# Performance work log

Measured on AMD Instinct MI355X. Metric: run time of the kernel, lower is better.

The kernel has to match this reference:

```python
import jax, jax.numpy as jnp
import numpy as np

B, C, O, H, W = 4, 64, 64, 128, 128
KH = KW = 3
K = KH * KW  # 9 kernel positions
MRM = 10.0   # max_residue_magnitude


def setup_inputs() -> dict:
    key = jax.random.key(0)
    ks = jax.random.split(key, 6)
    return {
        "x_main": jax.random.normal(ks[0], (B, C, H, W), jnp.float32),
        "x_extra": jax.random.normal(ks[1], (B, C, H, W), jnp.float32),
        "pre_offset": jax.random.normal(ks[2], (B, K, H, W, 2), jnp.float32) * 2.0,
        "pre_sim": jax.random.uniform(ks[3], (B, K, H, W), jnp.float32),
        "weight": jax.random.normal(ks[4], (O, C, KH, KW), jnp.float32) / np.sqrt(C * K),
        "bias": jnp.zeros((O,), jnp.float32),
        "w_om": jax.random.normal(ks[5], (3 * K, C, KH, KW), jnp.float32) * 0.01,
        "b_om": jnp.zeros((3 * K,), jnp.float32),
    }


def _bilinear(img, py, px):
    """img: [C,Hi,Wi]; py, px: [K,Ho,Wo] float sample coords. Zero padding outside."""
    Hi, Wi = img.shape[1], img.shape[2]
    y0 = jnp.floor(py)
    x0 = jnp.floor(px)
    dy = py - y0  # [K,Ho,Wo]
    dx = px - x0

    def gather(yi, xi):
        valid = ((yi >= 0) & (yi <= Hi - 1) & (xi >= 0) & (xi <= Wi - 1)).astype(img.dtype)
        yc = jnp.clip(yi, 0, Hi - 1).astype(jnp.int32)
        xc = jnp.clip(xi, 0, Wi - 1).astype(jnp.int32)
        return img[:, yc, xc] * valid[None]  # [C,K,Ho,Wo]

    v00 = gather(y0, x0)
    v01 = gather(y0, x0 + 1)
    v10 = gather(y0 + 1, x0)
    v11 = gather(y0 + 1, x0 + 1)
    return (v00 * (1 - dy) * (1 - dx) + v01 * (1 - dy) * dx
            + v10 * dy * (1 - dx) + v11 * dy * dx)


def reference(x_main, x_extra, pre_offset, pre_sim, weight, bias, w_om, b_om):
    # conv_offset_mask: 3x3, stride 1, pad 1 -> [B, 3K, H, W]
    out = jax.lax.conv_general_dilated(
        x_extra, w_om, (1, 1), ((1, 1), (1, 1)),
        dimension_numbers=("NCHW", "OIHW", "NCHW")) + b_om[None, :, None, None]
    o1, o2, mask = jnp.split(out, 3, axis=1)  # each [B,K,H,W]
    offset = MRM * jnp.tanh(jnp.concatenate([o1, o2], axis=1))  # [B,2K,H,W]
    # pre_offset reorder: even channels <- pre_offset[...,1] (y), odd <- pre_offset[...,0] (x)
    off_y = offset[:, 0::2] + pre_offset[..., 1]  # [B,K,H,W]
    off_x = offset[:, 1::2] + pre_offset[..., 0]
    mask = jax.nn.sigmoid(mask * pre_sim)  # use_sim=True

    f32 = offset.dtype
    ky = (jnp.arange(K) // KW).astype(f32)  # kernel row per position k
    kx = (jnp.arange(K) % KW).astype(f32)   # kernel col per position k
    # base grid: p = out_pos*stride - pad + k*dil = h - 1 + ky (stride=1,pad=1,dil=1)
    py = off_y + (jnp.arange(H, dtype=f32)[None, None, :, None] - 1.0) + ky[None, :, None, None]
    px = off_x + (jnp.arange(W, dtype=f32)[None, None, None, :] - 1.0) + kx[None, :, None, None]

    sampled = jax.vmap(_bilinear)(x_main, py, px)      # [B,C,K,H,W]
    sampled = sampled * mask[:, None]                   # modulated (DCNv2)
    y = jnp.einsum("bckhw,ock->bohw", sampled, weight.reshape(O, C, K))
    return y + bias[None, :, None, None]
```

## Files before the change

kernel.cpp:

```cpp
#include <hip/hip_runtime.h>
#include <math.h>

#define Bn 4
#define Cn 64
#define On 64
#define Hn 128
#define Wn 128
#define Kn 9
#define HWn (Hn*Wn)
#define ZROW 16384
#define XBSTRIDE (16385*64)

typedef _Float16 v8h __attribute__((ext_vector_type(8)));
typedef float v4f __attribute__((ext_vector_type(4)));

__device__ inline unsigned short f2h(float f) {
  _Float16 h = (_Float16)f;
  return __builtin_bit_cast(unsigned short, h);
}
__device__ inline _Float16 u2h(unsigned v) {
  return __builtin_bit_cast(_Float16, (unsigned short)(v & 0xffff));
}
__device__ inline v8h sp8(_Float16 x) { v8h v = {x,x,x,x,x,x,x,x}; return v; }

__device__ inline void gld_lds16(const void* g, void* s) {
  __builtin_amdgcn_global_load_lds(
      (const __attribute__((address_space(1))) unsigned int*)g,
      (__attribute__((address_space(3))) unsigned int*)s, 16, 0, 0);
}

__global__ __launch_bounds__(256) void k_prep(
    const float* __restrict__ x_main,
    const float* __restrict__ x_extra,
    const float* __restrict__ weight,
    const float* __restrict__ w_om,
    _Float16* __restrict__ xT,
    _Float16* __restrict__ xeF,
    _Float16* __restrict__ Wfrag,
    _Float16* __restrict__ WOMfrag)
{
  const int blk = blockIdx.x;
  const int t = threadIdx.x;

  if (blk < 2048) {
    __shared__ float tile[64 * 65];
    int isExtra = blk >> 10;
    int b  = (blk >> 8) & 3;
    int p0 = (blk & 255) << 6;
    const float* src = (isExtra ? x_extra : x_main) + b * Cn * HWn + p0;
    #pragma unroll
    for (int i = 0; i < 4; ++i) {
      int c  = i * 16 + (t >> 4);
      int p4 = (t & 15) * 4;
      float4 v = *(const float4*)(src + c * HWn + p4);
      tile[c * 65 + p4 + 0] = v.x;
      tile[c * 65 + p4 + 1] = v.y;
      tile[c * 65 + p4 + 2] = v.z;
      tile[c * 65 + p4 + 3] = v.w;
    }
    __syncthreads();
    _Float16* dst = (isExtra ? xeF : xT) + b * XBSTRIDE + p0 * 64;
    int q  = t & 7;
    int pr = t >> 3;
    #pragma unroll
    for (int i = 0; i < 2; ++i) {
      int p = i * 32 + pr;
      v8h pk;
      #pragma unroll
      for (int j = 0; j < 8; ++j)
        pk[j] = (_Float16)tile[(q * 8 + j) * 65 + p];
      *(v8h*)(dst + p * 64 + q * 8) = pk;
    }
  } else {
    int rb = blk - 2048;
    for (int idx = rb * 256 + t; idx < 36864; idx += 64 * 256) {
      int j  = idx & 7;
      int ln = (idx >> 3) & 63;
      int ot = (idx >> 9) & 3;
      int hk = (idx >> 11) & 1;
      int k  = idx >> 12;
      int o = ot * 16 + (ln & 15);
      int c = hk * 32 + (ln >> 4) * 8 + j;
      Wfrag[idx] = (_Float16)weight[(o * Cn + c) * Kn + k];
    }
    for (int idx = rb * 256 + t; idx < 18432; idx += 64 * 256) {
      int j    = idx & 7;
      int ln   = (idx >> 3) & 63;
      int jt   = (idx >> 9) & 1;
      int half = (idx >> 10) & 1;
      int k9   = idx >> 11;
      int jo = jt * 16 + (ln & 15);
      int c  = half * 32 + (ln >> 4) * 8 + j;
      float v = (jo < 27) ? w_om[(jo * Cn + c) * Kn + k9] : 0.f;
      WOMfrag[idx] = (_Float16)v;
    }
    if (rb == 0 && t < 256) {
      int b = t >> 6, c = t & 63;
      xT[b * XBSTRIDE + ZROW * 64 + c] = (_Float16)0.f;
      xeF[b * XBSTRIDE + ZROW * 64 + c] = (_Float16)0.f;
    }
  }
}

__global__ __launch_bounds__(256, 4) void k_fused(
    const _Float16* __restrict__ xT,
    const _Float16* __restrict__ xeF,
    const _Float16* __restrict__ Wfrag,
    const _Float16* __restrict__ WOMfrag,
    const float* __restrict__ pre_offset,
    const float* __restrict__ pre_sim,
    const float* __restrict__ b_om,
    const float* __restrict__ bias,
    float* __restrict__ out)
{
  __shared__ __align__(16) char smem[36864];

  const int t    = threadIdx.x;
  const int lane = t & 63;
  const int wv   = __builtin_amdgcn_readfirstlane(t >> 6);
  const int raw  = blockIdx.x;
  const int blk  = ((raw & 7) << 7) | (raw >> 3);
  const int b    = blk >> 8;
  const int h    = (blk >> 1) & 127;
  const int wq   = (blk & 1) * 4 + wv;
  const int kq   = lane >> 4;
  const int n    = lane & 15;
  const int w    = wq * 16 + n;

  unsigned tapoff[9];
  #pragma unroll
  for (int k9 = 0; k9 < 9; ++k9) {
    int r  = h - 1 + k9 / 3;
    int cc = w - 1 + k9 % 3;
    bool v = ((unsigned)r < (unsigned)Hn) & ((unsigned)cc < (unsigned)Wn);
    tapoff[k9] = (v ? (unsigned)(r * Wn + cc) : (unsigned)ZROW) * 64u;
  }

  const _Float16* xe = xeF + b * XBSTRIDE;
  v4f ca0 = {0,0,0,0}, ca1 = {0,0,0,0};

  {
    const v8h* WomV = (const v8h*)WOMfrag;
    #pragma unroll
    for (int f = 0; f < 9; ++f) {
      int id = wv * 9 + f;
      gld_lds16(WomV + id * 64 + lane, smem + id * 1024);
    }
  }
  __builtin_amdgcn_sched_barrier(0);
  v8h Bt0 = *(const v8h*)(xe + tapoff[0] + kq * 8);
  v8h Bt1 = *(const v8h*)(xe + tapoff[0] + 32 + kq * 8);
  asm volatile("s_waitcnt vmcnt(2)" ::: "memory");
  __builtin_amdgcn_s_barrier();

  #pragma unroll
  for (int k9 = 0; k9 < 9; ++k9) {
    v8h Bn0, Bn1;
    if (k9 < 8) {
      Bn0 = *(const v8h*)(xe + tapoff[k9 + 1] + kq * 8);
      Bn1 = *(const v8h*)(xe + tapoff[k9 + 1] + 32 + kq * 8);
    }
    __builtin_amdgcn_sched_barrier(0);
    const char* fb = smem + k9 * 4096 + lane * 16;
    v8h A00 = *(const v8h*)(fb);
    v8h A01 = *(const v8h*)(fb + 1024);
    ca0 = __builtin_amdgcn_mfma_f32_16x16x32_f16(A00, Bt0, ca0, 0, 0, 0);
    ca1 = __builtin_amdgcn_mfma_f32_16x16x32_f16(A01, Bt0, ca1, 0, 0, 0);
    v8h A10 = *(const v8h*)(fb + 2048);
    v8h A11 = *(const v8h*)(fb + 3072);
    ca0 = __builtin_amdgcn_mfma_f32_16x16x32_f16(A10, Bt1, ca0, 0, 0, 0);
    ca1 = __builtin_amdgcn_mfma_f32_16x16x32_f16(A11, Bt1, ca1, 0, 0, 0);
    if (k9 < 8) { Bt0 = Bn0; Bt1 = Bn1; }
  }
  __syncthreads();

  float* jb = (float*)smem + wv * 576;
  *(v4f*)(jb + n * 36 + kq * 4)      = ca0;
  *(v4f*)(jb + n * 36 + 16 + kq * 4) = ca1;

  const v8h* Wf = (const v8h*)Wfrag;
  char* AbufB = smem + 18432;
  if (wv == 0) {
    #pragma unroll
    for (int f = 0; f < 8; ++f)
      gld_lds16(Wf + f * 64 + lane, AbufB + f * 1024);
  }
  __builtin_amdgcn_sched_barrier(0);

  uint4* rb = (uint4*)(smem + 9216) + wv * 144;
  if (kq < 3) {
    #pragma unroll
    for (int kk = 0; kk < 3; ++kk) {
      int k = kq * 3 + kk;
      float sy = jb[n * 36 + 2 * k]     + b_om[2 * k];
      float sx = jb[n * 36 + 2 * k + 1] + b_om[2 * k + 1];
      float sm = jb[n * 36 + 18 + k]    + b_om[18 + k];
      int pbase = ((b * Kn + k) * Hn + h) * Wn + w;
      float2 po = *(const float2*)(pre_offset + pbase * 2);
      float ey = __expf(2.f * sy);
      float ex = __expf(2.f * sx);
      float py = 10.f - 20.f / (ey + 1.f) + po.y + (float)(h - 1 + k / 3);
      float px = 10.f - 20.f / (ex + 1.f) + po.x + (float)(w - 1 + k % 3);
      float m  = 1.f / (1.f + __expf(-sm * pre_sim[pbase]));
      float fy = floorf(py), fx = floorf(px);
      float dy = py - fy, dx = px - fx;
      int y0 = (int)fy, x0 = (int)fx;
      int y1 = y0 + 1, x1 = x0 + 1;
      bool vy0 = (y0 >= 0) & (y0 < Hn), vy1 = (y1 >= 0) & (y1 < Hn);
      bool vx0 = (x0 >= 0) & (x0 < Wn), vx1 = (x1 >= 0) & (x1 < Wn);
      unsigned r00 = (vy0 & vx0) ? (unsigned)(y0 * Wn + x0) : ZROW;
      unsigned r01 = (vy0 & vx1) ? (unsigned)(y0 * Wn + x1) : ZROW;
      unsigned r10 = (vy1 & vx0) ? (unsigned)(y1 * Wn + x0) : ZROW;
      unsigned r11 = (vy1 & vx1) ? (unsigned)(y1 * Wn + x1) : ZROW;
      float wy0 = 1.f - dy, wx0 = 1.f - dx;
      uint4 rec;
      rec.x = r00 | (r01 << 16);
      rec.y = r10 | (r11 << 16);
      rec.z = (unsigned)f2h(wy0 * wx0 * m) | ((unsigned)f2h(wy0 * dx * m) << 16);
      rec.w = (unsigned)f2h(dy * wx0 * m) | ((unsigned)f2h(dy * dx * m) << 16);
      rb[n * 9 + k] = rec;
    }
  }

  v4f acc0 = {0,0,0,0}, acc1 = {0,0,0,0}, acc2 = {0,0,0,0}, acc3 = {0,0,0,0};
  const _Float16* xb = xT + b * XBSTRIDE;

  uint4 rec0   = rb[n * 9 + 0];
  uint4 rec_nx = rb[n * 9 + 1];
  _Float16 h00 = u2h(rec0.z), h01 = u2h(rec0.z >> 16);
  _Float16 h10 = u2h(rec0.w), h11 = u2h(rec0.w >> 16);
  unsigned o00 = (rec0.x & 0xffff) * 64u + kq * 8;
  unsigned o01 = (rec0.x >> 16)    * 64u + kq * 8;
  unsigned o10 = (rec0.y & 0xffff) * 64u + kq * 8;
  unsigned o11 = (rec0.y >> 16)    * 64u + kq * 8;
  v8h C0 = *(const v8h*)(xb + o00);
  v8h C1 = *(const v8h*)(xb + o01);
  v8h C2 = *(const v8h*)(xb + o10);
  v8h C3 = *(const v8h*)(xb + o11);
  asm volatile("s_waitcnt vmcnt(4)" ::: "memory");
  __builtin_amdgcn_s_barrier();

  #pragma unroll
  for (int k = 0; k < 9; ++k) {
    if (k < 8 && wv == ((k + 1) & 3)) {
      #pragma unroll
      for (int f = 0; f < 8; ++f)
        gld_lds16(Wf + ((k + 1) * 8 + f) * 64 + lane,
                  AbufB + ((k + 1) & 1) * 8192 + f * 1024);
    }
    v8h H0 = *(const v8h*)(xb + o00 + 32);
    v8h H1 = *(const v8h*)(xb + o01 + 32);
    v8h H2 = *(const v8h*)(xb + o10 + 32);
    v8h H3 = *(const v8h*)(xb + o11 + 32);

    v8h N0, N1, N2, N3;
    _Float16 nh00 = (_Float16)0.f, nh01 = (_Float16)0.f;
    _Float16 nh10 = (_Float16)0.f, nh11 = (_Float16)0.f;
    unsigned p00 = 0, p01 = 0, p10 = 0, p11 = 0;
    if (k < 8) {
      nh00 = u2h(rec_nx.z); nh01 = u2h(rec_nx.z >> 16);
      nh10 = u2h(rec_nx.w); nh11 = u2h(rec_nx.w >> 16);
      p00 = (rec_nx.x & 0xffff) * 64u + kq * 8;
      p01 = (rec_nx.x >> 16)    * 64u + kq * 8;
      p10 = (rec_nx.y & 0xffff) * 64u + kq * 8;
      p11 = (rec_nx.y >> 16)    * 64u + kq * 8;
      N0 = *(const v8h*)(xb + p00);
      N1 = *(const v8h*)(xb + p01);
      N2 = *(const v8h*)(xb + p10);
      N3 = *(const v8h*)(xb + p11);
    }
    uint4 rec_nx2 = rec_nx;
    if (k < 7) rec_nx2 = rb[n * 9 + k + 2];

    __builtin_amdgcn_sched_barrier(0);

    const char* Ab = AbufB + (k & 1) * 8192 + lane * 16;
    v8h F0 = *(const v8h*)(Ab);
    v8h F1 = *(const v8h*)(Ab + 1024);
    v8h F2 = *(const v8h*)(Ab + 2048);
    v8h F3 = *(const v8h*)(Ab + 3072);

    v8h Bf0 = C0 * sp8(h00) + C1 * sp8(h01) + C2 * sp8(h10) + C3 * sp8(h11);

    acc0 = __builtin_amdgcn_mfma_f32_16x16x32_f16(F0, Bf0, acc0, 0, 0, 0);
    acc1 = __builtin_amdgcn_mfma_f32_16x16x32_f16(F1, Bf0, acc1, 0, 0, 0);
    acc2 = __builtin_amdgcn_mfma_f32_16x16x32_f16(F2, Bf0, acc2, 0, 0, 0);
    acc3 = __builtin_amdgcn_mfma_f32_16x16x32_f16(F3, Bf0, acc3, 0, 0, 0);

    v8h F4 = *(const v8h*)(Ab + 4096);
    v8h F5 = *(const v8h*)(Ab + 5120);
    v8h F6 = *(const v8h*)(Ab + 6144);
    v8h F7 = *(const v8h*)(Ab + 7168);
    v8h Bf1 = H0 * sp8(h00) + H1 * sp8(h01) + H2 * sp8(h10) + H3 * sp8(h11);

    acc0 = __builtin_amdgcn_mfma_f32_16x16x32_f16(F4, Bf1, acc0, 0, 0, 0);
    acc1 = __builtin_amdgcn_mfma_f32_16x16x32_f16(F5, Bf1, acc1, 0, 0, 0);
    acc2 = __builtin_amdgcn_mfma_f32_16x16x32_f16(F6, Bf1, acc2, 0, 0, 0);
    acc3 = __builtin_amdgcn_mfma_f32_16x16x32_f16(F7, Bf1, acc3, 0, 0, 0);

    if (k < 8) {
      C0 = N0; C1 = N1; C2 = N2; C3 = N3;
      h00 = nh00; h01 = nh01; h10 = nh10; h11 = nh11;
      o00 = p00; o01 = p01; o10 = p10; o11 = p11;
      rec_nx = rec_nx2;
      asm volatile("s_waitcnt vmcnt(4)" ::: "memory");
      __builtin_amdgcn_s_barrier();
    }
  }

  const float4* b4 = (const float4*)bias;
  float4 vb0 = b4[0 * 4 + kq], vb1 = b4[1 * 4 + kq];
  float4 vb2 = b4[2 * 4 + kq], vb3 = b4[3 * 4 + kq];
  float* ob = out + (b * On) * HWn + h * Wn + wq * 16 + n;
  #pragma unroll
  for (int reg = 0; reg < 4; ++reg) {
    ob[(0 * 16 + kq * 4 + reg) * HWn] = acc0[reg] + ((const float*)&vb0)[reg];
    ob[(1 * 16 + kq * 4 + reg) * HWn] = acc1[reg] + ((const float*)&vb1)[reg];
    ob[(2 * 16 + kq * 4 + reg) * HWn] = acc2[reg] + ((const float*)&vb2)[reg];
    ob[(3 * 16 + kq * 4 + reg) * HWn] = acc3[reg] + ((const float*)&vb3)[reg];
  }
}

extern "C" void kernel_launch(void* const* d_in, const int* in_sizes, int n_in,
                              void* d_out, int out_size, void* d_ws, size_t ws_size,
                              hipStream_t stream) {
  const float* x_main     = (const float*)d_in[0];
  const float* x_extra    = (const float*)d_in[1];
  const float* pre_offset = (const float*)d_in[2];
  const float* pre_sim    = (const float*)d_in[3];
  const float* weight     = (const float*)d_in[4];
  const float* bias       = (const float*)d_in[5];
  const float* w_om       = (const float*)d_in[6];
  const float* b_om       = (const float*)d_in[7];
  float* out = (float*)d_out;

  char* ws = (char*)d_ws;
  _Float16* xT      = (_Float16*)(ws);
  _Float16* xeF     = (_Float16*)(ws + 8389120);
  _Float16* Wfrag   = (_Float16*)(ws + 16778240);
  _Float16* WOMfrag = (_Float16*)(ws + 16851968);

  k_prep<<<2112, 256, 0, stream>>>(x_main, x_extra, weight, w_om,
                                   xT, xeF, Wfrag, WOMfrag);
  k_fused<<<1024, 256, 0, stream>>>(xT, xeF, Wfrag, WOMfrag,
                                    pre_offset, pre_sim, b_om, bias, out);
}
```

Baseline: 142.0 us.

## Split output channels across two blocks and shrink LDS for higher occupancy

Each block now computes only half of the output channels (32 of 64), doubling the grid to 2048 blocks. The offset-conv weight staging becomes a per-tap double buffer instead of preloading all taps, which halves LDS use and raises launch bounds to 8 blocks per CU. The aim is more resident waves to hide the latency of the irregular bilinear gathers. In exchange, each block redoes the offset/mask convolution and the bilinear sampling, and the next-tap prefetch of gathered pixels is replaced by waiting on vmcnt(0) every step.

```diff
diff --git a/kernel.cpp b/kernel.cpp
--- a/kernel.cpp
+++ b/kernel.cpp
@@ -102,7 +102,7 @@
   }
 }
 
-__global__ __launch_bounds__(256, 4) void k_fused(
+__global__ __launch_bounds__(256, 8) void k_fused(
     const _Float16* __restrict__ xT,
     const _Float16* __restrict__ xeF,
     const _Float16* __restrict__ Wfrag,
@@ -113,16 +113,18 @@
     const float* __restrict__ bias,
     float* __restrict__ out)
 {
-  __shared__ __align__(16) char smem[36864];
+  __shared__ __align__(16) char smem[18432];
 
   const int t    = threadIdx.x;
   const int lane = t & 63;
   const int wv   = __builtin_amdgcn_readfirstlane(t >> 6);
   const int raw  = blockIdx.x;
-  const int blk  = ((raw & 7) << 7) | (raw >> 3);
-  const int b    = blk >> 8;
-  const int h    = (blk >> 1) & 127;
-  const int wq   = (blk & 1) * 4 + wv;
+  const int blk  = ((raw & 7) << 8) | (raw >> 3);
+  const int oh   = blk & 1;
+  const int bh   = blk >> 1;
+  const int b    = bh >> 8;
+  const int h    = (bh >> 1) & 127;
+  const int wq   = (bh & 1) * 4 + wv;
   const int kq   = lane >> 4;
   const int n    = lane & 15;
   const int w    = wq * 16 + n;
@@ -137,16 +139,10 @@
   }
 
   const _Float16* xe = xeF + b * XBSTRIDE;
+  const v8h* WomV = (const v8h*)WOMfrag;
   v4f ca0 = {0,0,0,0}, ca1 = {0,0,0,0};
 
-  {
-    const v8h* WomV = (const v8h*)WOMfrag;
-    #pragma unroll
-    for (int f = 0; f < 9; ++f) {
-      int id = wv * 9 + f;
-      gld_lds16(WomV + id * 64 + lane, smem + id * 1024);
-    }
-  }
+  gld_lds16(WomV + (0 * 4 + wv) * 64 + lane, smem + wv * 1024);
   __builtin_amdgcn_sched_barrier(0);
   v8h Bt0 = *(const v8h*)(xe + tapoff[0] + kq * 8);
   v8h Bt1 = *(const v8h*)(xe + tapoff[0] + 32 + kq * 8);
@@ -155,13 +151,17 @@
 
   #pragma unroll
   for (int k9 = 0; k9 < 9; ++k9) {
+    if (k9 < 8)
+      gld_lds16(WomV + ((k9 + 1) * 4 + wv) * 64 + lane,
+                smem + ((k9 + 1) & 1) * 4096 + wv * 1024);
+    __builtin_amdgcn_sched_barrier(0);
     v8h Bn0, Bn1;
     if (k9 < 8) {
       Bn0 = *(const v8h*)(xe + tapoff[k9 + 1] + kq * 8);
       Bn1 = *(const v8h*)(xe + tapoff[k9 + 1] + 32 + kq * 8);
     }
     __builtin_amdgcn_sched_barrier(0);
-    const char* fb = smem + k9 * 4096 + lane * 16;
+    const char* fb = smem + (k9 & 1) * 4096 + lane * 16;
     v8h A00 = *(const v8h*)(fb);
     v8h A01 = *(const v8h*)(fb + 1024);
     ca0 = __builtin_amdgcn_mfma_f32_16x16x32_f16(A00, Bt0, ca0, 0, 0, 0);
@@ -170,22 +170,17 @@
     v8h A11 = *(const v8h*)(fb + 3072);
     ca0 = __builtin_amdgcn_mfma_f32_16x16x32_f16(A10, Bt1, ca0, 0, 0, 0);
     ca1 = __builtin_amdgcn_mfma_f32_16x16x32_f16(A11, Bt1, ca1, 0, 0, 0);
-    if (k9 < 8) { Bt0 = Bn0; Bt1 = Bn1; }
+    if (k9 < 8) {
+      Bt0 = Bn0; Bt1 = Bn1;
+      asm volatile("s_waitcnt vmcnt(2)" ::: "memory");
+      __builtin_amdgcn_s_barrier();
+    }
   }
   __syncthreads();
 
   float* jb = (float*)smem + wv * 576;
   *(v4f*)(jb + n * 36 + kq * 4)      = ca0;
   *(v4f*)(jb + n * 36 + 16 + kq * 4) = ca1;
-
-  const v8h* Wf = (const v8h*)Wfrag;
-  char* AbufB = smem + 18432;
-  if (wv == 0) {
-    #pragma unroll
-    for (int f = 0; f < 8; ++f)
-      gld_lds16(Wf + f * 64 + lane, AbufB + f * 1024);
-  }
-  __builtin_amdgcn_sched_barrier(0);
 
   uint4* rb = (uint4*)(smem + 9216) + wv * 144;
   if (kq < 3) {
@@ -221,103 +216,71 @@
       rb[n * 9 + k] = rec;
     }
   }
-
-  v4f acc0 = {0,0,0,0}, acc1 = {0,0,0,0}, acc2 = {0,0,0,0}, acc3 = {0,0,0,0};
+  __syncthreads();
+
+  v4f acc0 = {0,0,0,0}, acc1 = {0,0,0,0};
   const _Float16* xb = xT + b * XBSTRIDE;
-
-  uint4 rec0   = rb[n * 9 + 0];
-  uint4 rec_nx = rb[n * 9 + 1];
-  _Float16 h00 = u2h(rec0.z), h01 = u2h(rec0.z >> 16);
-  _Float16 h10 = u2h(rec0.w), h11 = u2h(rec0.w >> 16);
-  unsigned o00 = (rec0.x & 0xffff) * 64u + kq * 8;
-  unsigned o01 = (rec0.x >> 16)    * 64u + kq * 8;
-  unsigned o10 = (rec0.y & 0xffff) * 64u + kq * 8;
-  unsigned o11 = (rec0.y >> 16)    * 64u + kq * 8;
-  v8h C0 = *(const v8h*)(xb + o00);
-  v8h C1 = *(const v8h*)(xb + o01);
-  v8h C2 = *(const v8h*)(xb + o10);
-  v8h C3 = *(const v8h*)(xb + o11);
-  asm volatile("s_waitcnt vmcnt(4)" ::: "memory");
+  const v8h* Wf = (const v8h*)Wfrag;
+  const int fsel = (wv >> 1) * 4 + 2 * oh + (wv & 1);
+
+  gld_lds16(Wf + (0 * 8 + fsel) * 64 + lane, smem + wv * 1024);
+  __builtin_amdgcn_sched_barrier(0);
+  uint4 rec_cur = rb[n * 9 + 0];
+  asm volatile("s_waitcnt vmcnt(0)" ::: "memory");
   __builtin_amdgcn_s_barrier();
 
   #pragma unroll
   for (int k = 0; k < 9; ++k) {
-    if (k < 8 && wv == ((k + 1) & 3)) {
-      #pragma unroll
-      for (int f = 0; f < 8; ++f)
-        gld_lds16(Wf + ((k + 1) * 8 + f) * 64 + lane,
-                  AbufB + ((k + 1) & 1) * 8192 + f * 1024);
-    }
+    _Float16 h00 = u2h(rec_cur.z), h01 = u2h(rec_cur.z >> 16);
+    _Float16 h10 = u2h(rec_cur.w), h11 = u2h(rec_cur.w >> 16);
+    unsigned o00 = (rec_cur.x & 0xffff) * 64u + kq * 8;
+    unsigned o01 = (rec_cur.x >> 16)    * 64u + kq * 8;
+    unsigned o10 = (rec_cur.y & 0xffff) * 64u + kq * 8;
+    unsigned o11 = (rec_cur.y >> 16)    * 64u + kq * 8;
+    v8h C0 = *(const v8h*)(xb + o00);
+    v8h C1 = *(const v8h*)(xb + o01);
+    v8h C2 = *(const v8h*)(xb + o10);
+    v8h C3 = *(const v8h*)(xb + o11);
+    if (k < 8)
+      gld_lds16(Wf + ((k + 1) * 8 + fsel) * 64 + lane,
+                smem + ((k + 1) & 1) * 4096 + wv * 1024);
+    __builtin_amdgcn_sched_barrier(0);
+    uint4 rec_nx = rec_cur;
+    if (k < 8) rec_nx = rb[n * 9 + k + 1];
+
+    const char* Ab = smem + (k & 1) * 4096 + lane * 16;
+    v8h F0 = *(const v8h*)(Ab);
+    v8h F1 = *(const v8h*)(Ab + 1024);
+    v8h Bf0 = C0 * sp8(h00) + C1 * sp8(h01) + C2 * sp8(h10) + C3 * sp8(h11);
+    acc0 = __builtin_amdgcn_mfma_f32_16x16x32_f16(F0, Bf0, acc0, 0, 0, 0);
+    acc1 = __builtin_amdgcn_mfma_f32_16x16x32_f16(F1, Bf0, acc1, 0, 0, 0);
+
+    __builtin_amdgcn_sched_barrier(0);
     v8h H0 = *(const v8h*)(xb + o00 + 32);
     v8h H1 = *(const v8h*)(xb + o01 + 32);
     v8h H2 = *(const v8h*)(xb + o10 + 32);
     v8h H3 = *(const v8h*)(xb + o11 + 32);
-
-    v8h N0, N1, N2, N3;
-    _Float16 nh00 = (_Float16)0.f, nh01 = (_Float16)0.f;
-    _Float16 nh10 = (_Float16)0.f, nh11 = (_Float16)0.f;
-    unsigned p00 = 0, p01 = 0, p10 = 0, p11 = 0;
-    if (k < 8) {
-      nh00 = u2h(rec_nx.z); nh01 = u2h(rec_nx.z >> 16);
-      nh10 = u2h(rec_nx.w); nh11 = u2h(rec_nx.w >> 16);
-      p00 = (rec_nx.x & 0xffff) * 64u + kq * 8;
-      p01 = (rec_nx.x >> 16)    * 64u + kq * 8;
-      p10 = (rec_nx.y & 0xffff) * 64u + kq * 8;
-      p11 = (rec_nx.y >> 16)    * 64u + kq * 8;
-      N0 = *(const v8h*)(xb + p00);
-      N1 = *(const v8h*)(xb + p01);
-      N2 = *(const v8h*)(xb + p10);
-      N3 = *(const v8h*)(xb + p11);
-    }
-    uint4 rec_nx2 = rec_nx;
-    if (k < 7) rec_nx2 = rb[n * 9 + k + 2];
-
-    __builtin_amdgcn_sched_barrier(0);
-
-    const char* Ab = AbufB + (k & 1) * 8192 + lane * 16;
-    v8h F0 = *(const v8h*)(Ab);
-    v8h F1 = *(const v8h*)(Ab + 1024);
     v8h F2 = *(const v8h*)(Ab + 2048);
     v8h F3 = *(const v8h*)(Ab + 3072);
-
-    v8h Bf0 = C0 * sp8(h00) + C1 * sp8(h01) + C2 * sp8(h10) + C3 * sp8(h11);
-
-    acc0 = __builtin_amdgcn_mfma_f32_16x16x32_f16(F0, Bf0, acc0, 0, 0, 0);
-    acc1 = __builtin_amdgcn_mfma_f32_16x16x32_f16(F1, Bf0, acc1, 0, 0, 0);
-    acc2 = __builtin_amdgcn_mfma_f32_16x16x32_f16(F2, Bf0, acc2, 0, 0, 0);
-    acc3 = __builtin_amdgcn_mfma_f32_16x16x32_f16(F3, Bf0, acc3, 0, 0, 0);
-
-    v8h F4 = *(const v8h*)(Ab + 4096);
-    v8h F5 = *(const v8h*)(Ab + 5120);
-    v8h F6 = *(const v8h*)(Ab + 6144);
-    v8h F7 = *(const v8h*)(Ab + 7168);
     v8h Bf1 = H0 * sp8(h00) + H1 * sp8(h01) + H2 * sp8(h10) + H3 * sp8(h11);
-
-    acc0 = __builtin_amdgcn_mfma_f32_16x16x32_f16(F4, Bf1, acc0, 0, 0, 0);
-    acc1 = __builtin_amdgcn_mfma_f32_16x16x32_f16(F5, Bf1, acc1, 0, 0, 0);
-    acc2 = __builtin_amdgcn_mfma_f32_16x16x32_f16(F6, Bf1, acc2, 0, 0, 0);
-    acc3 = __builtin_amdgcn_mfma_f32_16x16x32_f16(F7, Bf1, acc3, 0, 0, 0);
-
+    acc0 = __builtin_amdgcn_mfma_f32_16x16x32_f16(F2, Bf1, acc0, 0, 0, 0);
+    acc1 = __builtin_amdgcn_mfma_f32_16x16x32_f16(F3, Bf1, acc1, 0, 0, 0);
+
+    rec_cur = rec_nx;
     if (k < 8) {
-      C0 = N0; C1 = N1; C2 = N2; C3 = N3;
-      h00 = nh00; h01 = nh01; h10 = nh10; h11 = nh11;
-      o00 = p00; o01 = p01; o10 = p10; o11 = p11;
-      rec_nx = rec_nx2;
-      asm volatile("s_waitcnt vmcnt(4)" ::: "memory");
+      asm volatile("s_waitcnt vmcnt(0)" ::: "memory");
       __builtin_amdgcn_s_barrier();
     }
   }
 
   const float4* b4 = (const float4*)bias;
-  float4 vb0 = b4[0 * 4 + kq], vb1 = b4[1 * 4 + kq];
-  float4 vb2 = b4[2 * 4 + kq], vb3 = b4[3 * 4 + kq];
-  float* ob = out + (b * On) * HWn + h * Wn + wq * 16 + n;
+  float4 vb0 = b4[(oh * 2 + 0) * 4 + kq];
+  float4 vb1 = b4[(oh * 2 + 1) * 4 + kq];
+  float* ob = out + (b * On + oh * 32) * HWn + h * Wn + wq * 16 + n;
   #pragma unroll
   for (int reg = 0; reg < 4; ++reg) {
     ob[(0 * 16 + kq * 4 + reg) * HWn] = acc0[reg] + ((const float*)&vb0)[reg];
     ob[(1 * 16 + kq * 4 + reg) * HWn] = acc1[reg] + ((const float*)&vb1)[reg];
-    ob[(2 * 16 + kq * 4 + reg) * HWn] = acc2[reg] + ((const float*)&vb2)[reg];
-    ob[(3 * 16 + kq * 4 + reg) * HWn] = acc3[reg] + ((const float*)&vb3)[reg];
   }
 }
 
@@ -342,6 +305,6 @@
 
   k_prep<<<2112, 256, 0, stream>>>(x_main, x_extra, weight, w_om,
                                    xT, xeF, Wfrag, WOMfrag);
-  k_fused<<<1024, 256, 0, stream>>>(xT, xeF, Wfrag, WOMfrag,
+  k_fused<<<2048, 256, 0, stream>>>(xT, xeF, Wfrag, WOMfrag,
                                     pre_offset, pre_sim, b_om, bias, out);
 }
```

Result: slower. 183.8 us (+29.4%).
